# Optimization experiments

Hardware: AMD Instinct MI355X
Metric: run time of the kernel (lower is better)

The kernel has to match this reference:

```python
import jax, jax.numpy as jnp
import numpy as np

T, D_IN, D_OUT, R, S = 8192, 4096, 4096, 16, 16  # tokens, in, out, lora rank, n_stacks
GATE_THRESHOLD = 0.12


def setup_inputs() -> dict:
    key = jax.random.key(0)
    ks = jax.random.split(key, 6)
    x = jax.random.normal(ks[0], (T, D_IN), jnp.float32)
    W = jax.random.normal(ks[1], (D_OUT, D_IN), jnp.float32) * 0.02  # frozen linear weight
    b = jax.random.normal(ks[2], (D_OUT,), jnp.float32) * 0.02       # frozen linear bias
    A = jax.random.normal(ks[3], (S, R, D_IN), jnp.float32) * 0.02   # per-stack lora_A
    B = jax.random.normal(ks[4], (S, D_OUT, R), jnp.float32) * 0.02  # per-stack lora_B
    domain_weights = jax.random.uniform(ks[5], (S,), jnp.float32)    # sigmoid-router weights per domain
    stack_domain = jnp.arange(S, dtype=jnp.int32)                    # stack -> domain index (count=1 each)
    return {"x": x, "W": W, "b": b, "A": A, "B": B,
            "domain_weights": domain_weights, "stack_domain": stack_domain}


def reference(x, W, b, A, B, domain_weights, stack_domain):
    # base frozen linear: out = x @ W^T + b
    base = x @ W.T + b  # [T, D_OUT]
    # threshold-gated per-stack weights: w if w > GATE_THRESHOLD else 0
    g = jnp.where(domain_weights > GATE_THRESHOLD, domain_weights, 0.0)[stack_domain]  # [S]
    # grouped LoRA: stack(x) = (x @ A_s^T) @ B_s^T, combined with gate weights
    h = jnp.einsum('td,srd->str', x, A)          # [S, T, R]
    lora = jnp.einsum('s,str,sor->to', g, h, B)  # [T, D_OUT]
    # original wraps stack contributions in torch.no_grad()
    return base + jax.lax.stop_gradient(lora)
```

## Files before the change

kernel.cpp:

```cpp
#include <hip/hip_runtime.h>
#include <hip/hip_bf16.h>

typedef __bf16 bf16;
typedef __attribute__((ext_vector_type(8))) __bf16 bf16x8;
typedef __attribute__((ext_vector_type(4))) float f32x4;

#define T_TOK 8192
#define DIN   4096
#define DOUT  4096
#define RNK   16
#define NS    16
#define KLORA (NS * RNK)
#define GATE  0.12f

typedef __attribute__((address_space(1))) const void gconst_t;
typedef __attribute__((address_space(3))) void lds_t;

__device__ __forceinline__ void gload_lds16(const void* g, void* l) {
  __builtin_amdgcn_global_load_lds((gconst_t*)g, (lds_t*)l, 16, 0, 0);
}

#define BAR() do { asm volatile("" ::: "memory"); \
                   __builtin_amdgcn_s_barrier();  \
                   asm volatile("" ::: "memory"); } while (0)
#define VMW(n) asm volatile("s_waitcnt vmcnt(" #n ")" ::: "memory")
#define LGKM(n) do { asm volatile("s_waitcnt lgkmcnt(" #n ")" ::: "memory"); \
                     __builtin_amdgcn_sched_barrier(0); } while (0)
#define SB0 __builtin_amdgcn_sched_barrier(0)

__global__ __launch_bounds__(256)
void prep_all_kernel(const float* __restrict__ x, bf16* __restrict__ xb,
                     const float* __restrict__ B, const float* __restrict__ dw,
                     const int* __restrict__ sd, bf16* __restrict__ bg,
                     const float* __restrict__ A, bf16* __restrict__ at) {
  __shared__ float tl[32][33];
  const int bid = blockIdx.x;
  if (bid < 16384) {
    const long i = ((long)bid * 256 + threadIdx.x) * 8;
    const float4 v0 = *(const float4*)(x + i);
    const float4 v1 = *(const float4*)(x + i + 4);
    bf16x8 o;
    o[0] = (bf16)v0.x; o[1] = (bf16)v0.y; o[2] = (bf16)v0.z; o[3] = (bf16)v0.w;
    o[4] = (bf16)v1.x; o[5] = (bf16)v1.y; o[6] = (bf16)v1.z; o[7] = (bf16)v1.w;
    *(bf16x8*)(xb + i) = o;
  } else if (bid < 16384 + 4096) {
    const int t = (bid - 16384) * 256 + threadIdx.x;
    const int o = t >> 8, k = t & 255, s = k >> 4, r = k & 15;
    const float w = dw[sd[s]];
    const float g = (w > GATE) ? w : 0.f;
    bg[t] = (bf16)(g * B[((size_t)s * DOUT + o) * RNK + r]);
  } else {
    const int tb = bid - 16384 - 4096;
    const int d0 = (tb & 127) * 32, k0 = (tb >> 7) * 32;
    const int tx = threadIdx.x & 31, ty = threadIdx.x >> 5;
#pragma unroll
    for (int i = 0; i < 32; i += 8)
      tl[ty + i][tx] = A[(size_t)(k0 + ty + i) * DIN + d0 + tx];
    __syncthreads();
#pragma unroll
    for (int i = 0; i < 32; i += 8)
      at[(size_t)(d0 + ty + i) * KLORA + k0 + tx] = (bf16)tl[tx][ty + i];
  }
}

__global__ __launch_bounds__(256)
void gemm_bt(const bf16* __restrict__ Am, const bf16* __restrict__ Bm,
             const float* __restrict__ extra, bf16* __restrict__ outB,
             int M, int N, int K) {
  constexpr int BM = 128, BN = 128, BK = 32;
  __shared__ __align__(16) bf16 At[BM * BK];
  __shared__ __align__(16) bf16 Bt[BN * BK];

  const int tid  = threadIdx.x;
  const int wave = tid >> 6, lane = tid & 63;

  const int nwg = gridDim.x, bid = blockIdx.x;
  const int qq  = nwg >> 3;
  const int sw  = (bid & 7) * qq + (bid >> 3);
  const int ntN = N / BN;
  const long row0 = (long)(sw / ntN) * BM;
  const long col0 = (long)(sw % ntN) * BN;

  f32x4 acc[4][4] = {};
  const int kSteps = K / BK;

  auto stage = [&](int ks) {
    const long k0 = (long)ks * BK;
#pragma unroll
    for (int r = 0; r < 2; ++r) {
      const int off = tid * 16 + r * 4096;
      const int row = off >> 6;
      const int el  = (off & 63) >> 1;
      char* ldsA = (char*)At + (wave << 10) + (r << 12);
      char* ldsB = (char*)Bt + (wave << 10) + (r << 12);
      gload_lds16(Am + (row0 + row) * K + k0 + el, ldsA);
      gload_lds16(Bm + (col0 + row) * K + k0 + el, ldsB);
    }
  };

  stage(0);
  for (int ks = 0; ks < kSteps; ++ks) {
    __syncthreads();
    bf16x8 afr[4], bfr[4];
    const int koff = (lane >> 4) << 3;
    const int rsel = lane & 15;
    const int wr = wave >> 1, wc = wave & 1;
#pragma unroll
    for (int m = 0; m < 4; ++m)
      afr[m] = *(const bf16x8*)&At[((wr << 6) + (m << 4) + rsel) * BK + koff];
#pragma unroll
    for (int n = 0; n < 4; ++n)
      bfr[n] = *(const bf16x8*)&Bt[((wc << 6) + (n << 4) + rsel) * BK + koff];
    __syncthreads();
    if (ks + 1 < kSteps) stage(ks + 1);
#pragma unroll
    for (int m = 0; m < 4; ++m)
#pragma unroll
      for (int n = 0; n < 4; ++n)
        acc[m][n] = __builtin_amdgcn_mfma_f32_16x16x32_bf16(afr[m], bfr[n],
                                                            acc[m][n], 0, 0, 0);
  }

  const int wr = wave >> 1, wc = wave & 1;
#pragma unroll
  for (int m = 0; m < 4; ++m)
#pragma unroll
    for (int n = 0; n < 4; ++n)
#pragma unroll
      for (int j = 0; j < 4; ++j) {
        const long row = row0 + wr * 64 + m * 16 + ((lane >> 4) << 2) + j;
        const long col = col0 + wc * 64 + n * 16 + (lane & 15);
        outB[row * N + col] = (bf16)(acc[m][n][j] + extra[row * N + col]);
      }
}

__global__ __launch_bounds__(512, 4)
void gemm256(const bf16* __restrict__ Am, const bf16* __restrict__ Bm,
             const float* __restrict__ bias, float* __restrict__ out,
             int M, int N, int K) {
  extern __shared__ char smem[];
  const int tid  = threadIdx.x;
  const int wave = tid >> 6, lane = tid & 63;
  const int wr = wave >> 2, wc = wave & 3;
  const int rsel = lane & 15, klane = lane >> 4;

  const int nwg = gridDim.x, bid = blockIdx.x;
  const int sw  = (bid & 7) * (nwg >> 3) + (bid >> 3);
  const int ntN = N >> 7;
  const long row0 = (long)(sw / ntN) << 8;
  const long col0 = (long)(sw % ntN) << 7;

  long srcA[2];
  int  ldsdA[2];
#pragma unroll
  for (int r = 0; r < 2; ++r) {
    const int row = wave * 32 + r * 16 + (lane >> 2);
    const int kbe = ((((lane & 3) * 16) ^ (lane & 32)) >> 1);
    srcA[r] = (row0 + row) * (long)K + kbe;
    ldsdA[r] = (wave * 2 + r) << 10;
  }
  const int rowB = tid >> 2;
  const int kbeB = ((((lane & 3) * 16) ^ (lane & 32)) >> 1);
  const long srcB = (col0 + rowB) * (long)K + kbeB;
  const int  ldsdB = wave << 10;

  const int nS = K >> 5;

  auto stageA = [&](int p, int s2) {
#pragma unroll
    for (int r = 0; r < 2; ++r)
      gload_lds16(Am + srcA[r] + (long)s2 * 32, smem + p * 24576 + ldsdA[r]);
  };
  auto stageB = [&](int p, int s2) {
    gload_lds16(Bm + srcB + (long)s2 * 32, smem + p * 24576 + 16384 + ldsdB);
  };

  const int laneoff = rsel * 64 + ((klane * 16) ^ ((rsel & 8) << 2));

  f32x4 acc[8][2] = {};
  bf16x8 afr[4], bfr[2];

#define RDA(p, mi, j) \
  afr[(j)] = *(const bf16x8*)(smem + (p) * 24576 + \
      (((wr << 7) + (mi) * 16) << 6) + laneoff)
#define RDB(p, n) \
  bfr[(n)] = *(const bf16x8*)(smem + (p) * 24576 + 16384 + \
      (((wc << 5) + (n) * 16) << 6) + laneoff)
#define MB(mi, j, n) \
  acc[(mi)][(n)] = __builtin_amdgcn_mfma_f32_16x16x32_bf16( \
      afr[(j)], bfr[(n)], acc[(mi)][(n)], 0, 0, 0)

  stageB(0, 0); stageA(0, 0);
  stageB(1, 1); stageA(1, 1);
  VMW(3);
  BAR();

  int p = 0, pst = 2;
  for (int s = 0; s < nS; ++s) {
    const bool more = (s + 2 < nS);
    RDB(p, 0); RDB(p, 1);
    RDA(p, 0, 0); RDA(p, 1, 1); RDA(p, 2, 2); RDA(p, 3, 3);
    if (more) stageB(pst, s + 2);
    BAR();
    LGKM(0);
    __builtin_amdgcn_s_setprio(1);
    MB(0, 0, 0); MB(0, 0, 1); MB(1, 1, 0); MB(1, 1, 1);
    MB(2, 2, 0); MB(2, 2, 1); MB(3, 3, 0); MB(3, 3, 1);
    __builtin_amdgcn_s_setprio(0);
    RDA(p, 4, 0); RDA(p, 5, 1); RDA(p, 6, 2); RDA(p, 7, 3);
    if (more) stageA(pst, s + 2);
    if (s >= nS - 2) { VMW(0); } else { VMW(3); }
    BAR();
    LGKM(0);
    __builtin_amdgcn_s_setprio(1);
    MB(4, 0, 0); MB(4, 0, 1); MB(5, 1, 0); MB(5, 1, 1);
    MB(6, 2, 0); MB(6, 2, 1); MB(7, 3, 0); MB(7, 3, 1);
    __builtin_amdgcn_s_setprio(0);
    p = (p == 2) ? 0 : p + 1;
    pst = (pst == 2) ? 0 : pst + 1;
  }

#undef RDA
#undef RDB
#undef MB

#pragma unroll
  for (int mi = 0; mi < 8; ++mi)
#pragma unroll
    for (int n = 0; n < 2; ++n)
#pragma unroll
      for (int j = 0; j < 4; ++j) {
        const long row = row0 + wr * 128 + mi * 16 + klane * 4 + j;
        const long col = col0 + wc * 32 + n * 16 + rsel;
        out[row * N + col] = acc[mi][n][j] + bias[col];
      }
}


extern "C" void kernel_launch(void* const* d_in, const int* in_sizes, int n_in,
                              void* d_out, int out_size, void* d_ws, size_t ws_size,
                              hipStream_t stream) {
  (void)in_sizes; (void)n_in; (void)out_size; (void)ws_size;
  const float* x  = (const float*)d_in[0];
  const float* W  = (const float*)d_in[1];
  const float* b  = (const float*)d_in[2];
  const float* A  = (const float*)d_in[3];
  const float* B  = (const float*)d_in[4];
  const float* dw = (const float*)d_in[5];
  const int*   sd = (const int*)d_in[6];
  float* out = (float*)d_out;

  char* ws = (char*)d_ws;
  bf16* xb    = (bf16*)(ws);
  bf16* weff  = (bf16*)(ws + ((size_t)64 << 20));
  bf16* bg    = (bf16*)(ws + ((size_t)96 << 20));
  bf16* acatT = (bf16*)(ws + ((size_t)98 << 20));

  prep_all_kernel<<<16384 + 4096 + 1024, 256, 0, stream>>>(
      x, xb, B, dw, sd, bg, A, acatT);

  gemm_bt<<<(DOUT / 128) * (DIN / 128), 256, 0, stream>>>(
      bg, acatT, W, weff, DOUT, DIN, KLORA);

  static_assert((T_TOK % 256) == 0 && (DOUT % 128) == 0 && (DIN % 32) == 0, "");
  hipFuncSetAttribute(reinterpret_cast<const void*>(gemm256),
                      hipFuncAttributeMaxDynamicSharedMemorySize, 73728);
  gemm256<<<(T_TOK / 256) * (DOUT / 128), 512, 73728, stream>>>(
      xb, weff, b, out, T_TOK, DOUT, DIN);
}
```

Before: 361.7 us.

## Enlarge main GEMM tile to 256x256 with 8-slot K=64 LDS pipeline

The main bf16 GEMM tile grows from 256x128 to 256x256 per workgroup, so each wave now holds an 8x4 accumulator block. Loads are staged in 64-wide K half-tiles through an 8-slot ring in 128KB of LDS, with a new XOR swizzle, and compute is interleaved in four quadrant phases per tile. The aim is to double the arithmetic done per byte loaded from global memory and LDS, and to hide load latency behind a deeper prefetch. In exchange, occupancy drops to 2 waves per SIMD, register pressure rises, the grid halves to 512 workgroups, and there are more barriers per tile.

```diff
diff --git a/kernel.cpp b/kernel.cpp
--- a/kernel.cpp
+++ b/kernel.cpp
@@ -27,6 +27,8 @@
 #define LGKM(n) do { asm volatile("s_waitcnt lgkmcnt(" #n ")" ::: "memory"); \
                      __builtin_amdgcn_sched_barrier(0); } while (0)
 #define SB0 __builtin_amdgcn_sched_barrier(0)
+#define PRIO1 __builtin_amdgcn_s_setprio(1)
+#define PRIO0 __builtin_amdgcn_s_setprio(0)
 
 __global__ __launch_bounds__(256)
 void prep_all_kernel(const float* __restrict__ x, bf16* __restrict__ xb,
@@ -134,7 +136,7 @@
       }
 }
 
-__global__ __launch_bounds__(512, 4)
+__global__ __launch_bounds__(512, 2)
 void gemm256(const bf16* __restrict__ Am, const bf16* __restrict__ Bm,
              const float* __restrict__ bias, float* __restrict__ out,
              int M, int N, int K) {
@@ -146,93 +148,123 @@
 
   const int nwg = gridDim.x, bid = blockIdx.x;
   const int sw  = (bid & 7) * (nwg >> 3) + (bid >> 3);
-  const int ntN = N >> 7;
+  const int ntN = N >> 8;
   const long row0 = (long)(sw / ntN) << 8;
-  const long col0 = (long)(sw % ntN) << 7;
-
-  long srcA[2];
-  int  ldsdA[2];
+  const long col0 = (long)(sw % ntN) << 8;
+
+  long srcA[2], srcB[2];
+  int  ldsd[2];
 #pragma unroll
   for (int r = 0; r < 2; ++r) {
-    const int row = wave * 32 + r * 16 + (lane >> 2);
-    const int kbe = ((((lane & 3) * 16) ^ (lane & 32)) >> 1);
-    srcA[r] = (row0 + row) * (long)K + kbe;
-    ldsdA[r] = (wave * 2 + r) << 10;
+    const int chunk = wave * 2 + r;
+    const int rowl  = chunk * 8 + (lane >> 3);
+    const int kbe   = ((lane & 7) ^ ((lane >> 3) & 7)) << 3;
+    srcA[r] = (row0 + rowl) * (long)K + kbe;
+    srcB[r] = (col0 + rowl) * (long)K + kbe;
+    ldsd[r] = chunk << 10;
   }
-  const int rowB = tid >> 2;
-  const int kbeB = ((((lane & 3) * 16) ^ (lane & 32)) >> 1);
-  const long srcB = (col0 + rowB) * (long)K + kbeB;
-  const int  ldsdB = wave << 10;
-
-  const int nS = K >> 5;
-
-  auto stageA = [&](int p, int s2) {
-#pragma unroll
-    for (int r = 0; r < 2; ++r)
-      gload_lds16(Am + srcA[r] + (long)s2 * 32, smem + p * 24576 + ldsdA[r]);
+
+  const int nT = K >> 6;
+  const int nIter = nT >> 1;
+
+  auto stageH = [&](int H) {
+    if (H >= 4 * nT) return;
+    const int  slot = H & 7;
+    const long ofs  = ((H & 2) ? 128L * K : 0L) + (long)(H >> 2) * 64;
+    char* dst = smem + (slot << 14);
+    if (H & 1) {
+      gload_lds16(Bm + srcB[0] + ofs, dst + ldsd[0]);
+      gload_lds16(Bm + srcB[1] + ofs, dst + ldsd[1]);
+    } else {
+      gload_lds16(Am + srcA[0] + ofs, dst + ldsd[0]);
+      gload_lds16(Am + srcA[1] + ofs, dst + ldsd[1]);
+    }
   };
-  auto stageB = [&](int p, int s2) {
-    gload_lds16(Bm + srcB + (long)s2 * 32, smem + p * 24576 + 16384 + ldsdB);
-  };
-
-  const int laneoff = rsel * 64 + ((klane * 16) ^ ((rsel & 8) << 2));
-
-  f32x4 acc[8][2] = {};
-  bf16x8 afr[4], bfr[2];
-
-#define RDA(p, mi, j) \
-  afr[(j)] = *(const bf16x8*)(smem + (p) * 24576 + \
-      (((wr << 7) + (mi) * 16) << 6) + laneoff)
-#define RDB(p, n) \
-  bfr[(n)] = *(const bf16x8*)(smem + (p) * 24576 + 16384 + \
-      (((wc << 5) + (n) * 16) << 6) + laneoff)
-#define MB(mi, j, n) \
-  acc[(mi)][(n)] = __builtin_amdgcn_mfma_f32_16x16x32_bf16( \
-      afr[(j)], bfr[(n)], acc[(mi)][(n)], 0, 0, 0)
-
-  stageB(0, 0); stageA(0, 0);
-  stageB(1, 1); stageA(1, 1);
-  VMW(3);
+
+  const int sAofs = 2 * wr;
+  const int sBofs = 1 + 2 * (wc >> 1);
+  const int brow  = (wc & 1) * 64;
+
+  f32x4 acc[8][4] = {};
+  bf16x8 afr[4][2];
+  bf16x8 bfr[2][2][2];
+
+#define RDA(T, mh, mi, kst) \
+  afr[mi][kst] = *(const bf16x8*)(smem + ((((4 * (T)) + sAofs) & 7) << 14) \
+      + ((mh) * 64 + (mi) * 16 + rsel) * 128 \
+      + ((((kst) * 64) + klane * 16) ^ ((rsel & 7) << 4)))
+#define RDB(T, nh, ni, kst) \
+  bfr[nh][ni][kst] = *(const bf16x8*)(smem + ((((4 * (T)) + sBofs) & 7) << 14) \
+      + (brow + (nh) * 32 + (ni) * 16 + rsel) * 128 \
+      + ((((kst) * 64) + klane * 16) ^ ((rsel & 7) << 4)))
+#define MQ(mh, nh) do { \
+  _Pragma("unroll") for (int _k = 0; _k < 2; ++_k) \
+    _Pragma("unroll") for (int _m = 0; _m < 4; ++_m) \
+      _Pragma("unroll") for (int _n = 0; _n < 2; ++_n) \
+        acc[(mh) * 4 + _m][(nh) * 2 + _n] = \
+            __builtin_amdgcn_mfma_f32_16x16x32_bf16( \
+                afr[_m][_k], bfr[nh][_n][_k], \
+                acc[(mh) * 4 + _m][(nh) * 2 + _n], 0, 0, 0); \
+} while (0)
+
+  stageH(0); stageH(1); stageH(2); stageH(3);
+  VMW(4);
+  stageH(4); stageH(5); stageH(6);
+  VMW(6);
   BAR();
 
-  int p = 0, pst = 2;
-  for (int s = 0; s < nS; ++s) {
-    const bool more = (s + 2 < nS);
-    RDB(p, 0); RDB(p, 1);
-    RDA(p, 0, 0); RDA(p, 1, 1); RDA(p, 2, 2); RDA(p, 3, 3);
-    if (more) stageB(pst, s + 2);
-    BAR();
-    LGKM(0);
-    __builtin_amdgcn_s_setprio(1);
-    MB(0, 0, 0); MB(0, 0, 1); MB(1, 1, 0); MB(1, 1, 1);
-    MB(2, 2, 0); MB(2, 2, 1); MB(3, 3, 0); MB(3, 3, 1);
-    __builtin_amdgcn_s_setprio(0);
-    RDA(p, 4, 0); RDA(p, 5, 1); RDA(p, 6, 2); RDA(p, 7, 3);
-    if (more) stageA(pst, s + 2);
-    if (s >= nS - 2) { VMW(0); } else { VMW(3); }
-    BAR();
-    LGKM(0);
-    __builtin_amdgcn_s_setprio(1);
-    MB(4, 0, 0); MB(4, 0, 1); MB(5, 1, 0); MB(5, 1, 1);
-    MB(6, 2, 0); MB(6, 2, 1); MB(7, 3, 0); MB(7, 3, 1);
-    __builtin_amdgcn_s_setprio(0);
-    p = (p == 2) ? 0 : p + 1;
-    pst = (pst == 2) ? 0 : pst + 1;
+  for (int u = 0; u < nIter; ++u) {
+    const int Ta = 2 * u, Tb = 2 * u + 1;
+    const int H0 = 8 * u;
+    const bool lastIt = (u == nIter - 1);
+
+#define TILE4(T, Hbase) do { \
+     \
+    RDA(T, 0, 0, 0); RDA(T, 0, 0, 1); RDA(T, 0, 1, 0); RDA(T, 0, 1, 1); \
+    RDA(T, 0, 2, 0); RDA(T, 0, 2, 1); RDA(T, 0, 3, 0); RDA(T, 0, 3, 1); \
+    RDB(T, 0, 0, 0); RDB(T, 0, 0, 1); RDB(T, 0, 1, 0); RDB(T, 0, 1, 1); \
+    stageH((Hbase)); \
+    BAR(); LGKM(0); \
+    PRIO1; MQ(0, 0); PRIO0; \
+    BAR(); \
+     \
+    RDB(T, 1, 0, 0); RDB(T, 1, 0, 1); RDB(T, 1, 1, 0); RDB(T, 1, 1, 1); \
+    BAR(); LGKM(0); \
+    PRIO1; MQ(0, 1); PRIO0; \
+    BAR(); \
+     \
+    RDA(T, 1, 0, 0); RDA(T, 1, 0, 1); RDA(T, 1, 1, 0); RDA(T, 1, 1, 1); \
+    RDA(T, 1, 2, 0); RDA(T, 1, 2, 1); RDA(T, 1, 3, 0); RDA(T, 1, 3, 1); \
+    stageH((Hbase) + 2); \
+    BAR(); LGKM(0); \
+    PRIO1; MQ(1, 0); PRIO0; \
+    BAR(); \
+     \
+    stageH((Hbase) + 1); stageH((Hbase) + 3); \
+    BAR(); \
+    PRIO1; MQ(1, 1); PRIO0; \
+    if (lastIt) { VMW(0); } else { VMW(6); } \
+    BAR(); \
+} while (0)
+
+    TILE4(Ta, H0 + 7);
+    TILE4(Tb, H0 + 11);
+#undef TILE4
   }
 
 #undef RDA
 #undef RDB
-#undef MB
-
-#pragma unroll
-  for (int mi = 0; mi < 8; ++mi)
-#pragma unroll
-    for (int n = 0; n < 2; ++n)
+#undef MQ
+
+#pragma unroll
+  for (int am = 0; am < 8; ++am)
+#pragma unroll
+    for (int an = 0; an < 4; ++an)
 #pragma unroll
       for (int j = 0; j < 4; ++j) {
-        const long row = row0 + wr * 128 + mi * 16 + klane * 4 + j;
-        const long col = col0 + wc * 32 + n * 16 + rsel;
-        out[row * N + col] = acc[mi][n][j] + bias[col];
+        const long row = row0 + wr * 128 + am * 16 + klane * 4 + j;
+        const long col = col0 + wc * 64 + an * 16 + rsel;
+        out[row * N + col] = acc[am][an][j] + bias[col];
       }
 }
 
@@ -262,9 +294,9 @@
   gemm_bt<<<(DOUT / 128) * (DIN / 128), 256, 0, stream>>>(
       bg, acatT, W, weff, DOUT, DIN, KLORA);
 
-  static_assert((T_TOK % 256) == 0 && (DOUT % 128) == 0 && (DIN % 32) == 0, "");
+  static_assert((T_TOK % 256) == 0 && (DOUT % 256) == 0 && (DIN % 128) == 0, "");
   hipFuncSetAttribute(reinterpret_cast<const void*>(gemm256),
-                      hipFuncAttributeMaxDynamicSharedMemorySize, 73728);
-  gemm256<<<(T_TOK / 256) * (DOUT / 128), 512, 73728, stream>>>(
+                      hipFuncAttributeMaxDynamicSharedMemorySize, 131072);
+  gemm256<<<(T_TOK / 256) * (DOUT / 256), 512, 131072, stream>>>(
       xb, weff, b, out, T_TOK, DOUT, DIN);
 }
```

New measurement: 305.8 us, median of 3. 15.5% less time.
